# Kernel tuning notes

Hardware: AMD Instinct MI355X
Metric: run time of the kernel (lower is better)

The kernel has to match this reference:

```python
import jax, jax.numpy as jnp
import numpy as np

BITS = 4
MAXQ = (1 << BITS) - 1          # 15
PACK = 32 // BITS               # 8 values per int32
IN_F = 4096
OUT_F = 11008


def setup_inputs() -> dict:
    key = jax.random.key(0)
    k1, k2, k3, k4, k5 = jax.random.split(key, 5)
    x = jax.random.normal(k1, (8, IN_F), dtype=jnp.float32)
    qweight = jax.random.randint(k2, (IN_F // 32 * BITS, OUT_F), 0, 2147483647, dtype=jnp.int32)
    qzeros = jax.random.randint(k3, (1, OUT_F // 32 * BITS), 0, 2147483647, dtype=jnp.int32)
    scales = jax.random.uniform(k4, (1, OUT_F), dtype=jnp.float32, minval=1e-3, maxval=2e-2)
    bias = jax.random.normal(k5, (OUT_F,), dtype=jnp.float32)
    return {"x": x, "qweight": qweight, "qzeros": qzeros, "scales": scales, "bias": bias}


def reference(x, qweight, qzeros, scales, bias):
    # GPTQ-style unpack: each int32 packs PACK values of BITS bits, LSB first.
    shifts = jnp.arange(0, 32, BITS, dtype=jnp.int32)  # wf
    # unpack weights: (IN_F//PACK, OUT_F) -> (IN_F//PACK, PACK, OUT_F) -> (IN_F, OUT_F)
    w = (qweight[:, None, :] >> shifts[None, :, None]) & MAXQ
    w = w.reshape(IN_F, OUT_F).astype(scales.dtype)
    # unpack zeros: (1, OUT_F//PACK) -> (1, OUT_F//PACK, PACK) -> (1, OUT_F), +1 per GPTQ convention
    z = ((qzeros[:, :, None] >> shifts[None, None, :]) & MAXQ) + 1
    z = z.reshape(1, OUT_F).astype(scales.dtype)
    # single quantization group (group_size == infeatures, g_idx all zeros)
    W = scales * (w - z)                      # (IN_F, OUT_F)
    return x @ W + bias
```

## Files before the change

kernel.cpp:

```cpp
#include <hip/hip_runtime.h>

#define IN_F 4096
#define OUT_F 11008
#define M 8
#define S_SLICES 16
#define KPS (IN_F / S_SLICES)
#define RPSL (KPS / 8)
#define STEPS (KPS / 32)

typedef __bf16 bf16x8 __attribute__((ext_vector_type(8)));
typedef float  f32x4  __attribute__((ext_vector_type(4)));
typedef unsigned short us8 __attribute__((ext_vector_type(8)));

__device__ __forceinline__ float trunc_bf(float v) {
    return __uint_as_float(__float_as_uint(v) & 0xffff0000u);
}

__global__ __launch_bounds__(64) void rowsum_kernel(
    const float* __restrict__ x, float* __restrict__ rs)
{
    const int r = blockIdx.x, t = threadIdx.x;
    const float4* xp = (const float4*)(x + (size_t)r * IN_F);
    float s = 0.0f;
#pragma unroll
    for (int c = 0; c < 16; ++c) {
        float4 v = xp[c * 64 + t];
        s += trunc_bf(v.x) + trunc_bf(v.y) + trunc_bf(v.z) + trunc_bf(v.w);
    }
#pragma unroll
    for (int off = 1; off < 64; off <<= 1) s += __shfl_xor(s, off, 64);
    if (t == 0) rs[r] = s;
}

__global__ __launch_bounds__(256) void convert_x_kernel(
    const float* __restrict__ x, unsigned short* __restrict__ xb)
{
    const int idx = blockIdx.x * 256 + threadIdx.x;
    const int r = idx >> 9;
    const int c = (idx & 511) * 8;
    us8 o;
    if (r < M) {
        const float4 v0 = *(const float4*)(x + (size_t)r * IN_F + c);
        const float4 v1 = *(const float4*)(x + (size_t)r * IN_F + c + 4);
        o[0] = (unsigned short)(__float_as_uint(v0.x) >> 16);
        o[1] = (unsigned short)(__float_as_uint(v0.y) >> 16);
        o[2] = (unsigned short)(__float_as_uint(v0.z) >> 16);
        o[3] = (unsigned short)(__float_as_uint(v0.w) >> 16);
        o[4] = (unsigned short)(__float_as_uint(v1.x) >> 16);
        o[5] = (unsigned short)(__float_as_uint(v1.y) >> 16);
        o[6] = (unsigned short)(__float_as_uint(v1.z) >> 16);
        o[7] = (unsigned short)(__float_as_uint(v1.w) >> 16);
    } else {
        o = (us8)0;
    }
    *(us8*)(xb + (size_t)r * IN_F + c) = o;
}

__global__ __launch_bounds__(256) void gptq_mfma_kernel(
    const int* __restrict__ qw,
    const unsigned short* __restrict__ xb,
    float* __restrict__ P)
{
    const int lane = threadIdx.x & 63;
    const int wv   = threadIdx.x >> 6;
    const int t    = lane & 15;
    const int quad = lane >> 4;
    const int col  = (blockIdx.x * 4 + wv) * 16 + t;
    const int i0   = blockIdx.y * RPSL;
    const int kb   = blockIdx.y * KPS;

    int    qv [STEPS];
    bf16x8 afr[STEPS];
    const int* qcol = qw + (size_t)(i0 + quad) * OUT_F + col;
    const unsigned short* xrow = xb + (size_t)t * IN_F + kb + quad * 8;
#pragma unroll
    for (int s = 0; s < STEPS; ++s) {
        qv[s]  = qcol[(size_t)s * 4 * OUT_F];
        afr[s] = *(const bf16x8*)(xrow + s * 32);
    }

    f32x4 acc = {0.f, 0.f, 0.f, 0.f};
#pragma unroll
    for (int s = 0; s < STEPS; ++s) {
        union { unsigned short u[8]; bf16x8 v; } bf;
#pragma unroll
        for (int j = 0; j < 8; ++j) {
            const float f = (float)((qv[s] >> (4 * j)) & 15);
            bf.u[j] = (unsigned short)(__float_as_uint(f) >> 16);
        }
        acc = __builtin_amdgcn_mfma_f32_16x16x32_bf16(afr[s], bf.v, acc, 0, 0, 0);
    }

    const int r0 = quad * 4;
    if (r0 < M) {
        float* Pp = P + (size_t)blockIdx.y * (M * OUT_F);
#pragma unroll
        for (int r = 0; r < 4; ++r)
            Pp[(size_t)(r0 + r) * OUT_F + col] = acc[r];
    }
}

__global__ __launch_bounds__(256) void reduce_kernel(
    const float* __restrict__ P, const float* __restrict__ rs,
    const int* __restrict__ qz, const float* __restrict__ sc,
    const float* __restrict__ bias, float* __restrict__ out)
{
    const int idx = blockIdx.x * 256 + threadIdx.x;
    const int j = idx % OUT_F;
    const int r = idx / OUT_F;

    float acc = 0.0f;
#pragma unroll
    for (int s = 0; s < S_SLICES; ++s)
        acc += P[(size_t)s * M * OUT_F + (size_t)r * OUT_F + j];

    const int zw = qz[j >> 3];
    const float z = (float)(((zw >> ((j & 7) * 4)) & 15) + 1);
    out[(size_t)r * OUT_F + j] = fmaf(sc[j], acc - z * rs[r], bias[j]);
}

extern "C" void kernel_launch(void* const* d_in, const int* in_sizes, int n_in,
                              void* d_out, int out_size, void* d_ws, size_t ws_size,
                              hipStream_t stream) {
    const float* x    = (const float*)d_in[0];
    const int*   qw   = (const int*)d_in[1];
    const int*   qz   = (const int*)d_in[2];
    const float* sc   = (const float*)d_in[3];
    const float* bias = (const float*)d_in[4];
    float* out = (float*)d_out;

    float*          P  = (float*)d_ws;
    unsigned short* xb = (unsigned short*)((char*)d_ws + (8u << 20));
    float*          rs = (float*)((char*)d_ws + (16u << 20));

    hipLaunchKernelGGL(rowsum_kernel, dim3(M), dim3(64), 0, stream, x, rs);
    hipLaunchKernelGGL(convert_x_kernel, dim3(32), dim3(256), 0, stream, x, xb);
    hipLaunchKernelGGL(gptq_mfma_kernel, dim3(OUT_F / 64, S_SLICES), dim3(256), 0, stream,
                       qw, xb, P);
    hipLaunchKernelGGL(reduce_kernel, dim3((M * OUT_F) / 256), dim3(256), 0, stream,
                       P, rs, qz, sc, bias, out);
}
```

Measured before the change: 90.35 us.

## Fuse x conversion and zero-point subtraction into MFMA kernel, drop prep kernels

Removes the rowsum and x-to-bf16 conversion kernels. The GEMM kernel now reads fp32 x directly and packs it to bf16 in registers. The zero point is subtracted from each weight nibble before conversion, so the epilogue only applies scale and bias. This cuts two kernel launches and the workspace round trip for the converted x. In exchange, the x conversion is repeated in every block and the weight dequant does slightly more integer work per nibble.

```diff
diff --git a/kernel.cpp b/kernel.cpp
--- a/kernel.cpp
+++ b/kernel.cpp
@@ -10,56 +10,17 @@
 
 typedef __bf16 bf16x8 __attribute__((ext_vector_type(8)));
 typedef float  f32x4  __attribute__((ext_vector_type(4)));
-typedef unsigned short us8 __attribute__((ext_vector_type(8)));
+typedef unsigned int u32x4 __attribute__((ext_vector_type(4)));
 
-__device__ __forceinline__ float trunc_bf(float v) {
-    return __uint_as_float(__float_as_uint(v) & 0xffff0000u);
-}
-
-__global__ __launch_bounds__(64) void rowsum_kernel(
-    const float* __restrict__ x, float* __restrict__ rs)
-{
-    const int r = blockIdx.x, t = threadIdx.x;
-    const float4* xp = (const float4*)(x + (size_t)r * IN_F);
-    float s = 0.0f;
-#pragma unroll
-    for (int c = 0; c < 16; ++c) {
-        float4 v = xp[c * 64 + t];
-        s += trunc_bf(v.x) + trunc_bf(v.y) + trunc_bf(v.z) + trunc_bf(v.w);
-    }
-#pragma unroll
-    for (int off = 1; off < 64; off <<= 1) s += __shfl_xor(s, off, 64);
-    if (t == 0) rs[r] = s;
-}
-
-__global__ __launch_bounds__(256) void convert_x_kernel(
-    const float* __restrict__ x, unsigned short* __restrict__ xb)
-{
-    const int idx = blockIdx.x * 256 + threadIdx.x;
-    const int r = idx >> 9;
-    const int c = (idx & 511) * 8;
-    us8 o;
-    if (r < M) {
-        const float4 v0 = *(const float4*)(x + (size_t)r * IN_F + c);
-        const float4 v1 = *(const float4*)(x + (size_t)r * IN_F + c + 4);
-        o[0] = (unsigned short)(__float_as_uint(v0.x) >> 16);
-        o[1] = (unsigned short)(__float_as_uint(v0.y) >> 16);
-        o[2] = (unsigned short)(__float_as_uint(v0.z) >> 16);
-        o[3] = (unsigned short)(__float_as_uint(v0.w) >> 16);
-        o[4] = (unsigned short)(__float_as_uint(v1.x) >> 16);
-        o[5] = (unsigned short)(__float_as_uint(v1.y) >> 16);
-        o[6] = (unsigned short)(__float_as_uint(v1.z) >> 16);
-        o[7] = (unsigned short)(__float_as_uint(v1.w) >> 16);
-    } else {
-        o = (us8)0;
-    }
-    *(us8*)(xb + (size_t)r * IN_F + c) = o;
+__device__ __forceinline__ unsigned pack_bf(float lo, float hi) {
+    return (__float_as_uint(lo) >> 16) | (__float_as_uint(hi) & 0xffff0000u);
 }
 
 __global__ __launch_bounds__(256) void gptq_mfma_kernel(
-    const int* __restrict__ qw,
-    const unsigned short* __restrict__ xb,
-    float* __restrict__ P)
+    const float* __restrict__ x,
+    const int*   __restrict__ qw,
+    const int*   __restrict__ qz,
+    float*       __restrict__ P)
 {
     const int lane = threadIdx.x & 63;
     const int wv   = threadIdx.x >> 6;
@@ -69,26 +30,42 @@
     const int i0   = blockIdx.y * RPSL;
     const int kb   = blockIdx.y * KPS;
 
-    int    qv [STEPS];
-    bf16x8 afr[STEPS];
+    const int zi = ((qz[col >> 3] >> ((col & 7) * 4)) & 15) + 1;
+
+    int qv[STEPS];
     const int* qcol = qw + (size_t)(i0 + quad) * OUT_F + col;
-    const unsigned short* xrow = xb + (size_t)t * IN_F + kb + quad * 8;
+#pragma unroll
+    for (int s = 0; s < STEPS; ++s)
+        qv[s] = qcol[(size_t)s * 4 * OUT_F];
+
+    union AF { u32x4 u; bf16x8 v; } afr[STEPS];
+    const float* xrow = x + (size_t)t * IN_F + kb + quad * 8;
 #pragma unroll
     for (int s = 0; s < STEPS; ++s) {
-        qv[s]  = qcol[(size_t)s * 4 * OUT_F];
-        afr[s] = *(const bf16x8*)(xrow + s * 32);
+        if (t < M) {
+            const float4 a = *(const float4*)(xrow + s * 32);
+            const float4 b = *(const float4*)(xrow + s * 32 + 4);
+            afr[s].u[0] = pack_bf(a.x, a.y);
+            afr[s].u[1] = pack_bf(a.z, a.w);
+            afr[s].u[2] = pack_bf(b.x, b.y);
+            afr[s].u[3] = pack_bf(b.z, b.w);
+        } else {
+            afr[s].u = (u32x4)(0u);
+        }
     }
 
     f32x4 acc = {0.f, 0.f, 0.f, 0.f};
 #pragma unroll
     for (int s = 0; s < STEPS; ++s) {
-        union { unsigned short u[8]; bf16x8 v; } bf;
+        union { u32x4 u; bf16x8 v; } bf;
+        const int q = qv[s];
 #pragma unroll
-        for (int j = 0; j < 8; ++j) {
-            const float f = (float)((qv[s] >> (4 * j)) & 15);
-            bf.u[j] = (unsigned short)(__float_as_uint(f) >> 16);
+        for (int w = 0; w < 4; ++w) {
+            const int n0 = ((q >> (8 * w))     & 15) - zi;
+            const int n1 = ((q >> (8 * w + 4)) & 15) - zi;
+            bf.u[w] = pack_bf((float)n0, (float)n1);
         }
-        acc = __builtin_amdgcn_mfma_f32_16x16x32_bf16(afr[s], bf.v, acc, 0, 0, 0);
+        acc = __builtin_amdgcn_mfma_f32_16x16x32_bf16(afr[s].v, bf.v, acc, 0, 0, 0);
     }
 
     const int r0 = quad * 4;
@@ -100,9 +77,8 @@
     }
 }
 
-__global__ __launch_bounds__(256) void reduce_kernel(
-    const float* __restrict__ P, const float* __restrict__ rs,
-    const int* __restrict__ qz, const float* __restrict__ sc,
+__global__ __launch_bounds__(256) void epilogue_kernel(
+    const float* __restrict__ P, const float* __restrict__ sc,
     const float* __restrict__ bias, float* __restrict__ out)
 {
     const int idx = blockIdx.x * 256 + threadIdx.x;
@@ -114,9 +90,7 @@
     for (int s = 0; s < S_SLICES; ++s)
         acc += P[(size_t)s * M * OUT_F + (size_t)r * OUT_F + j];
 
-    const int zw = qz[j >> 3];
-    const float z = (float)(((zw >> ((j & 7) * 4)) & 15) + 1);
-    out[(size_t)r * OUT_F + j] = fmaf(sc[j], acc - z * rs[r], bias[j]);
+    out[(size_t)r * OUT_F + j] = fmaf(sc[j], acc, bias[j]);
 }
 
 extern "C" void kernel_launch(void* const* d_in, const int* in_sizes, int n_in,
@@ -129,14 +103,10 @@
     const float* bias = (const float*)d_in[4];
     float* out = (float*)d_out;
 
-    float*          P  = (float*)d_ws;
-    unsigned short* xb = (unsigned short*)((char*)d_ws + (8u << 20));
-    float*          rs = (float*)((char*)d_ws + (16u << 20));
+    float* P = (float*)d_ws;
 
-    hipLaunchKernelGGL(rowsum_kernel, dim3(M), dim3(64), 0, stream, x, rs);
-    hipLaunchKernelGGL(convert_x_kernel, dim3(32), dim3(256), 0, stream, x, xb);
     hipLaunchKernelGGL(gptq_mfma_kernel, dim3(OUT_F / 64, S_SLICES), dim3(256), 0, stream,
-                       qw, xb, P);
-    hipLaunchKernelGGL(reduce_kernel, dim3((M * OUT_F) / 256), dim3(256), 0, stream,
-                       P, rs, qz, sc, bias, out);
+                       x, qw, qz, P);
+    hipLaunchKernelGGL(epilogue_kernel, dim3((M * OUT_F) / 256), dim3(256), 0, stream,
+                       P, sc, bias, out);
 }
```

After: 93.92 us. 1.04x slower.
